# Kernel optimization log

Measured on AMD Instinct MI355X. Metric: run time of the kernel, lower is better.

Reference implementation:

```python
import jax, jax.numpy as jnp
import numpy as np

N_NODES = 100000
N_EDGES = 800000
NUM_GRAPHS = 512
IN_DIM = 16
EDGE_DIM = 1
HID = 64       # emb_dim
MLP_H = 32     # hidden_layers inside each MPNNLayer
L = 3          # num_layers
EPS = 1e-5


def setup_inputs() -> dict:
    key = jax.random.key(0)
    ks = jax.random.split(key, 24)
    s = 0.05
    inp = {
        "x": jax.random.normal(ks[0], (N_NODES, IN_DIM), jnp.float32),
        "edge_index": jax.random.randint(ks[1], (2, N_EDGES), 0, N_NODES),
        "edge_attr": jax.random.uniform(ks[2], (N_EDGES, EDGE_DIM), jnp.float32),
        "batch": jnp.sort(jax.random.randint(ks[3], (N_NODES,), 0, NUM_GRAPHS)),
        # input projection
        "lin_in_w": jax.random.normal(ks[4], (IN_DIM, HID), jnp.float32) * s,
        "lin_in_b": jnp.zeros((HID,), jnp.float32),
        # message MLP (stacked over L layers): Linear(129->32), BN(32), ReLU, Linear(32->64), ReLU, BN(64)
        "msg_w1": jax.random.normal(ks[5], (L, 2 * HID + EDGE_DIM, MLP_H), jnp.float32) * s,
        "msg_b1": jnp.zeros((L, MLP_H), jnp.float32),
        "msg_g1": jnp.ones((L, MLP_H), jnp.float32),
        "msg_be1": jnp.zeros((L, MLP_H), jnp.float32),
        "msg_w2": jax.random.normal(ks[6], (L, MLP_H, HID), jnp.float32) * s,
        "msg_b2": jnp.zeros((L, HID), jnp.float32),
        "msg_g2": jnp.ones((L, HID), jnp.float32),
        "msg_be2": jnp.zeros((L, HID), jnp.float32),
        # update MLP: Linear(128->32), BN(32), ReLU, Linear(32->64), ReLU, BN(64)
        "upd_w1": jax.random.normal(ks[7], (L, 2 * HID, MLP_H), jnp.float32) * s,
        "upd_b1": jnp.zeros((L, MLP_H), jnp.float32),
        "upd_g1": jnp.ones((L, MLP_H), jnp.float32),
        "upd_be1": jnp.zeros((L, MLP_H), jnp.float32),
        "upd_w2": jax.random.normal(ks[8], (L, MLP_H, HID), jnp.float32) * s,
        "upd_b2": jnp.zeros((L, HID), jnp.float32),
        "upd_g2": jnp.ones((L, HID), jnp.float32),
        "upd_be2": jnp.zeros((L, HID), jnp.float32),
        # head Linear(64->1) + ReLU
        "out_w": jax.random.normal(ks[9], (HID, 1), jnp.float32) * s,
        "out_b": jnp.zeros((1,), jnp.float32),
    }
    return inp


def _bn(h, g, b):
    # BatchNorm1d, training-mode batch stats (biased variance), dropout treated as identity (eval)
    mu = jnp.mean(h, axis=0)
    var = jnp.var(h, axis=0)
    return g * (h - mu) * jax.lax.rsqrt(var + EPS) + b


def reference(x, edge_index, edge_attr, batch,
              lin_in_w, lin_in_b,
              msg_w1, msg_b1, msg_g1, msg_be1, msg_w2, msg_b2, msg_g2, msg_be2,
              upd_w1, upd_b1, upd_g1, upd_be1, upd_w2, upd_b2, upd_g2, upd_be2,
              out_w, out_b):
    src = edge_index[0]  # x_j source
    dst = edge_index[1]  # x_i target / aggregation index
    h = x @ lin_in_w + lin_in_b  # [N, HID]
    for l in range(L):
        # message: cat([x_i, x_j, edge_attr]) -> Linear -> BN -> ReLU -> Linear -> ReLU -> BN
        m_in = jnp.concatenate([h[dst], h[src], edge_attr], axis=1)  # [E, 2*HID+EDGE_DIM]
        m = jax.nn.relu(_bn(m_in @ msg_w1[l] + msg_b1[l], msg_g1[l], msg_be1[l]))
        m = _bn(jax.nn.relu(m @ msg_w2[l] + msg_b2[l]), msg_g2[l], msg_be2[l])
        # aggregate: scatter-add over destination nodes
        agg = jax.ops.segment_sum(m, dst, num_segments=N_NODES)  # [N, HID]
        # update: cat([x, aggr]) -> Linear -> BN -> ReLU -> Linear -> ReLU -> BN
        u_in = jnp.concatenate([h, agg], axis=1)  # [N, 2*HID]
        u = jax.nn.relu(_bn(u_in @ upd_w1[l] + upd_b1[l], upd_g1[l], upd_be1[l]))
        u = _bn(jax.nn.relu(u @ upd_w2[l] + upd_b2[l]), upd_g2[l], upd_be2[l])
        h = h + u  # residual (x += conv(...))
    # global mean pool
    pooled = jax.ops.segment_sum(h, batch, num_segments=NUM_GRAPHS)
    counts = jax.ops.segment_sum(jnp.ones((h.shape[0],), h.dtype), batch, num_segments=NUM_GRAPHS)
    pooled = pooled / jnp.maximum(counts, 1.0)[:, None]
    return jax.nn.relu(pooled @ out_w + out_b).reshape(-1)  # [NUM_GRAPHS]
```

## Files before the change

kernel.cpp:

```cpp
#include <hip/hip_runtime.h>
#include <hip/hip_bf16.h>

#define N_NODES   100000
#define N_EDGES   800000
#define NUM_GRAPHS 512
#define IN_DIM    16
#define HID       64
#define MLP_H     32
#define EPS       1e-5f
#define TPB       256
#define SCAN_B    1024
#define NCHUNK    ((N_NODES + SCAN_B - 1) / SCAN_B)
#define GSB       2048
#define NWAVES    (GSB * 4)
#define PER_W     ((N_EDGES + NWAVES - 1) / NWAVES)
#define NODEBLKS  ((N_NODES + 63) / 64)

using nh2   = decltype(__builtin_amdgcn_cvt_pkrtz(0.f, 0.f));
typedef _Float16 f16x8 __attribute__((ext_vector_type(8)));
typedef float    f32x4 __attribute__((ext_vector_type(4)));
typedef int      i32x4 __attribute__((ext_vector_type(4)));

__device__ __forceinline__ nh2 pack2(float a, float b) {
  return __builtin_amdgcn_cvt_pkrtz(a, b);
}
__device__ __forceinline__ float wsum(float v) {
  v += __shfl_xor(v, 1, 64);
  v += __shfl_xor(v, 2, 64);
  v += __shfl_xor(v, 4, 64);
  v += __shfl_xor(v, 8, 64);
  v += __shfl_xor(v, 16, 64);
  v += __shfl_xor(v, 32, 64);
  return v;
}
__device__ __forceinline__ int lbound(const int* __restrict__ rs, int key) {
  int lo = 0, hi = N_NODES;
  while (lo < hi) { int m = (lo + hi) >> 1; if (rs[m] < key) lo = m + 1; else hi = m; }
  return lo;
}

__global__ __launch_bounds__(TPB) void k_deg(const int* __restrict__ ei, int* __restrict__ deg) {
  int e = blockIdx.x * TPB + threadIdx.x;
  if (e < N_EDGES) atomicAdd(&deg[ei[N_EDGES + e]], 1);
}

__global__ __launch_bounds__(SCAN_B) void k_scan_part(const int* __restrict__ deg,
                                                      int* __restrict__ partials) {
  __shared__ int red[SCAN_B];
  int i = blockIdx.x * SCAN_B + threadIdx.x;
  red[threadIdx.x] = (i < N_NODES) ? deg[i] : 0;
  __syncthreads();
  for (int off = SCAN_B / 2; off > 0; off >>= 1) {
    if (threadIdx.x < off) red[threadIdx.x] += red[threadIdx.x + off];
    __syncthreads();
  }
  if (threadIdx.x == 0) partials[blockIdx.x] = red[0];
}

__global__ void k_scan_mid(int* __restrict__ partials, int* __restrict__ row_start) {
  int run = 0;
  for (int b = 0; b < NCHUNK; ++b) { int t = partials[b]; partials[b] = run; run += t; }
  row_start[N_NODES] = run;
}

__global__ __launch_bounds__(SCAN_B) void k_scan_fin(const int* __restrict__ deg,
                                                     const int* __restrict__ partials,
                                                     int* __restrict__ row_start,
                                                     int* __restrict__ cursor) {
  __shared__ int buf[2][SCAN_B];
  int t = threadIdx.x, i = blockIdx.x * SCAN_B + t;
  int v = (i < N_NODES) ? deg[i] : 0;
  buf[0][t] = v;
  __syncthreads();
  int cur = 0;
  for (int off = 1; off < SCAN_B; off <<= 1) {
    int nv = buf[cur][t] + ((t >= off) ? buf[cur][t - off] : 0);
    buf[cur ^ 1][t] = nv; cur ^= 1;
    __syncthreads();
  }
  if (i < N_NODES) {
    int excl = buf[cur][t] - v + partials[blockIdx.x];
    row_start[i] = excl;
    cursor[i] = excl;
  }
}

__global__ __launch_bounds__(TPB) void k_fill(const int* __restrict__ ei,
                                              const float* __restrict__ ea,
                                              int* __restrict__ cursor,
                                              int* __restrict__ srcS,
                                              int* __restrict__ dstS,
                                              float* __restrict__ eaS) {
  int e = blockIdx.x * TPB + threadIdx.x;
  if (e >= N_EDGES) return;
  int dst = ei[N_EDGES + e];
  int pos = atomicAdd(&cursor[dst], 1);
  srcS[pos] = ei[e];
  dstS[pos] = dst;
  eaS[pos] = ea[e];
}

__global__ __launch_bounds__(TPB) void k_lin_in(const float* __restrict__ x,
                                                const float* __restrict__ w,
                                                const float* __restrict__ b,
                                                float* __restrict__ h) {
  int i = blockIdx.x * TPB + threadIdx.x;
  if (i >= N_NODES) return;
  float xi[IN_DIM];
  const float4* xp = reinterpret_cast<const float4*>(x + i * IN_DIM);
#pragma unroll
  for (int q = 0; q < 4; ++q) {
    float4 v = xp[q];
    xi[4*q] = v.x; xi[4*q+1] = v.y; xi[4*q+2] = v.z; xi[4*q+3] = v.w;
  }
  float4* hp = reinterpret_cast<float4*>(h + i * HID);
#pragma unroll
  for (int j4 = 0; j4 < HID/4; ++j4) {
    float o[4];
#pragma unroll
    for (int c = 0; c < 4; ++c) {
      int j = j4*4 + c;
      float acc = b[j];
#pragma unroll
      for (int k = 0; k < IN_DIM; ++k) acc += xi[k] * w[k*HID + j];
      o[c] = acc;
    }
    float4 ov = {o[0], o[1], o[2], o[3]};
    hp[j4] = ov;
  }
}

__global__ __launch_bounds__(TPB) void k_pq(const float* __restrict__ h,
                                            const float* __restrict__ w1,
                                            const float* __restrict__ b1,
                                            float* __restrict__ P,
                                            _Float16* __restrict__ Qh) {
  const int part = __builtin_amdgcn_readfirstlane(threadIdx.x >> 6);
  const int lane = threadIdx.x & 63;
  const int i = blockIdx.x * 64 + lane;
  if (i >= N_NODES) return;
  const int jb = (part & 1) * 16;
  const bool isQ = part >= 2;
  const float* wbase = w1 + (isQ ? 64 * MLP_H : 0) + jb;
  float acc[16];
#pragma unroll
  for (int j = 0; j < 16; ++j) acc[j] = isQ ? 0.f : b1[jb + j];
  const float4* hp = reinterpret_cast<const float4*>(h + i * HID);
#pragma unroll 4
  for (int k4 = 0; k4 < 16; ++k4) {
    float4 a = hp[k4];
    const float* wr = wbase + (k4*4) * MLP_H;
#pragma unroll
    for (int j = 0; j < 16; ++j)
      acc[j] += a.x*wr[j] + a.y*wr[MLP_H+j] + a.z*wr[2*MLP_H+j] + a.w*wr[3*MLP_H+j];
  }
  if (!isQ) {
    float4* pp = reinterpret_cast<float4*>(P + i * MLP_H + jb);
#pragma unroll
    for (int c = 0; c < 4; ++c) {
      float4 o = {acc[4*c], acc[4*c+1], acc[4*c+2], acc[4*c+3]};
      pp[c] = o;
    }
  } else {
    i32x4 o0, o1;
#pragma unroll
    for (int c = 0; c < 4; ++c) {
      o0[c] = __builtin_bit_cast(int, pack2(acc[2*c],     acc[2*c+1]));
      o1[c] = __builtin_bit_cast(int, pack2(acc[8+2*c],   acc[8+2*c+1]));
    }
    i32x4* qp = reinterpret_cast<i32x4*>(Qh + i * MLP_H + jb);
    qp[0] = o0; qp[1] = o1;
  }
}

__global__ __launch_bounds__(TPB) void k_gather(const float* __restrict__ P,
                                                const _Float16* __restrict__ Qh,
                                                const int* __restrict__ srcS,
                                                const int* __restrict__ dstS,
                                                const float* __restrict__ eaS,
                                                const float* __restrict__ w1,
                                                _Float16* __restrict__ z1h,
                                                float* __restrict__ gstat) {
  const int lane = threadIdx.x & 63;
  const int k = lane & 31;
  const int half = lane >> 5;
  const float weak = w1[128 * MLP_H + k];
  float s = 0.f, q = 0.f;
  const int wv = blockIdx.x * 4 + (threadIdx.x >> 6);
  const int c0 = wv * PER_W;
  const int c1 = min(c0 + PER_W, N_EDGES);
  if (c0 < N_EDGES) {
    const int rounds = (c1 - c0 + 1) >> 1;
    const int e0 = c0 + half;
    int ea0 = min(e0, c1 - 1);
    int ea1 = min(e0 + 2, c1 - 1);
    float aA = eaS[ea0], aB = eaS[ea1];
    float qA = (float)Qh[srcS[ea0] * MLP_H + k], qB = (float)Qh[srcS[ea1] * MLP_H + k];
    float pA = P[dstS[ea0] * MLP_H + k], pB = P[dstS[ea1] * MLP_H + k];
    for (int r = 0; r < rounds; ++r) {
      const int ecur = e0 + 2 * r;
      const bool vc = ecur < c1;
      const int ecl = min(ecur, c1 - 1);
      float z = pA + qA + aA * weak;
      pA = pB; qA = qB; aA = aB;
      const int en = min(e0 + 2 * (r + 2), c1 - 1);
      aB = eaS[en]; qB = (float)Qh[srcS[en] * MLP_H + k]; pB = P[dstS[en] * MLP_H + k];
      if (vc) {
        z1h[ecl * MLP_H + k] = (_Float16)z;
        s += z; q = fmaf(z, z, q);
      }
    }
  }
  s += __shfl_xor(s, 32, 64);
  q += __shfl_xor(q, 32, 64);
  __shared__ float ls[4][MLP_H], lq[4][MLP_H];
  const int w = threadIdx.x >> 6;
  if (lane < MLP_H) { ls[w][lane] = s; lq[w][lane] = q; }
  __syncthreads();
  const int t = threadIdx.x;
  if (t < MLP_H)
    unsafeAtomicAdd(&gstat[t], ls[0][t] + ls[1][t] + ls[2][t] + ls[3][t]);
  else if (t < 2*MLP_H)
    unsafeAtomicAdd(&gstat[t], lq[0][t-MLP_H] + lq[1][t-MLP_H] + lq[2][t-MLP_H] + lq[3][t-MLP_H]);
}

__global__ __launch_bounds__(TPB) void k_msgdot(const _Float16* __restrict__ z1h,
                                                const int* __restrict__ rs,
                                                const float* __restrict__ gstat_in,
                                                const float* __restrict__ g1,
                                                const float* __restrict__ be1,
                                                const float* __restrict__ w2,
                                                const float* __restrict__ b2,
                                                float* __restrict__ agg,
                                                float* __restrict__ gstat_out) {
  const int lane = threadIdx.x & 63;
  const int col = lane & 15;
  const int g   = lane >> 4;
  float a1v[8], c1v[8];
#pragma unroll
  for (int i = 0; i < 8; ++i) {
    int kf = g*8 + i;
    float mu = gstat_in[kf] * (1.f / N_EDGES);
    float var = fmaxf(gstat_in[MLP_H + kf] * (1.f / N_EDGES) - mu * mu, 0.f);
    float a = g1[kf] * rsqrtf(var + EPS);
    a1v[i] = a; c1v[i] = be1[kf] - a * mu;
  }
  f16x8 bf0, bf1, bf2, bf3;
#define MKB(BF, C) { i32x4 bw; \
  _Pragma("unroll") for (int ii = 0; ii < 4; ++ii) { \
    nh2 p = pack2(w2[(g*8 + 2*ii) * HID + (C)*16 + col], \
                  w2[(g*8 + 2*ii + 1) * HID + (C)*16 + col]); \
    bw[ii] = __builtin_bit_cast(int, p); } \
  BF = __builtin_bit_cast(f16x8, bw); }
  MKB(bf0, 0) MKB(bf1, 1) MKB(bf2, 2) MKB(bf3, 3)
#undef MKB
  float b2c[4];
#pragma unroll
  for (int c = 0; c < 4; ++c) b2c[c] = b2[c*16 + col];

  float sacc[4] = {0.f,0.f,0.f,0.f}, qacc[4] = {0.f,0.f,0.f,0.f};
  const int wv = blockIdx.x * 4 + (threadIdx.x >> 6);
  const int key0 = min(wv * PER_W, N_EDGES);
  const int key1 = min((wv + 1) * PER_W, N_EDGES);
  const int n0 = lbound(rs, key0);
  const int n1 = (wv == NWAVES - 1) ? N_NODES : lbound(rs, key1);

  for (int n = n0; n < n1; ++n) {
    const int start = rs[n], end = rs[n + 1];
    float aggacc[4] = {0.f,0.f,0.f,0.f};
    for (int t0 = start; t0 < end; t0 += 16) {
      const int ec = min(t0 + col, end - 1);
      f16x8 zv = *reinterpret_cast<const f16x8*>(z1h + ec * MLP_H + g * 8);
      i32x4 aw;
#pragma unroll
      for (int i = 0; i < 4; ++i) {
        float m0 = fmaxf(fmaf(a1v[2*i],   (float)zv[2*i],   c1v[2*i]),   0.f);
        float m1 = fmaxf(fmaf(a1v[2*i+1], (float)zv[2*i+1], c1v[2*i+1]), 0.f);
        aw[i] = __builtin_bit_cast(int, pack2(m0, m1));
      }
      f16x8 af = __builtin_bit_cast(f16x8, aw);
      f32x4 zc = {0.f,0.f,0.f,0.f};
      f32x4 cc0 = __builtin_amdgcn_mfma_f32_16x16x32_f16(af, bf0, zc, 0, 0, 0);
      f32x4 cc1 = __builtin_amdgcn_mfma_f32_16x16x32_f16(af, bf1, zc, 0, 0, 0);
      f32x4 cc2 = __builtin_amdgcn_mfma_f32_16x16x32_f16(af, bf2, zc, 0, 0, 0);
      f32x4 cc3 = __builtin_amdgcn_mfma_f32_16x16x32_f16(af, bf3, zc, 0, 0, 0);
      bool vld[4];
#pragma unroll
      for (int reg = 0; reg < 4; ++reg) vld[reg] = (t0 + g*4 + reg) < end;
#define EPI(CC, CI) { \
  _Pragma("unroll") for (int reg = 0; reg < 4; ++reg) { \
    float tv = fmaxf(CC[reg] + b2c[CI], 0.f); \
    tv = vld[reg] ? tv : 0.f; \
    aggacc[CI] += tv; qacc[CI] = fmaf(tv, tv, qacc[CI]); } }
      EPI(cc0, 0) EPI(cc1, 1) EPI(cc2, 2) EPI(cc3, 3)
#undef EPI
    }
#pragma unroll
    for (int c = 0; c < 4; ++c) sacc[c] += aggacc[c];
#pragma unroll
    for (int c = 0; c < 4; ++c) {
      aggacc[c] += __shfl_xor(aggacc[c], 16, 64);
      aggacc[c] += __shfl_xor(aggacc[c], 32, 64);
    }
    float aout = (g == 0) ? aggacc[0] : (g == 1) ? aggacc[1] : (g == 2) ? aggacc[2] : aggacc[3];
    agg[n * HID + g * 16 + col] = aout;
  }
#pragma unroll
  for (int c = 0; c < 4; ++c) {
    sacc[c] += __shfl_xor(sacc[c], 16, 64);
    sacc[c] += __shfl_xor(sacc[c], 32, 64);
    qacc[c] += __shfl_xor(qacc[c], 16, 64);
    qacc[c] += __shfl_xor(qacc[c], 32, 64);
  }
  __shared__ float ls[4][HID], lq[4][HID];
  const int w = threadIdx.x >> 6;
  if (g == 0) {
#pragma unroll
    for (int c = 0; c < 4; ++c) { ls[w][c*16 + col] = sacc[c]; lq[w][c*16 + col] = qacc[c]; }
  }
  __syncthreads();
  const int t = threadIdx.x;
  if (t < HID)
    unsafeAtomicAdd(&gstat_out[t], ls[0][t] + ls[1][t] + ls[2][t] + ls[3][t]);
  else if (t < 2*HID)
    unsafeAtomicAdd(&gstat_out[t], lq[0][t-HID] + lq[1][t-HID] + lq[2][t-HID] + lq[3][t-HID]);
}

__global__ __launch_bounds__(TPB) void k_upd1(const float* __restrict__ h,
                                              const float* __restrict__ agg,
                                              const int* __restrict__ deg,
                                              const float* __restrict__ gstat_in,
                                              const float* __restrict__ g2,
                                              const float* __restrict__ be2,
                                              const float* __restrict__ w1,
                                              const float* __restrict__ b1,
                                              float* __restrict__ zu1) {
  __shared__ float sa[HID], sc[HID];
  {
    int t = threadIdx.x;
    if (t < HID) {
      float mu = gstat_in[t] * (1.f / N_EDGES);
      float var = fmaxf(gstat_in[HID + t] * (1.f / N_EDGES) - mu * mu, 0.f);
      float a = g2[t] * rsqrtf(var + EPS);
      sa[t] = a; sc[t] = be2[t] - a * mu;
    }
  }
  __syncthreads();
  const int widx = __builtin_amdgcn_readfirstlane(threadIdx.x >> 6);
  const int part = widx & 1;
  const int grp  = blockIdx.x * 2 + (widx >> 1);
  const int lane = threadIdx.x & 63;
  const int jb = part * 16;
  const int i = grp * 64 + lane;
  if (i >= N_NODES) return;
  float acc[16];
#pragma unroll
  for (int j = 0; j < 16; ++j) acc[j] = b1[jb + j];
  const float4* hp = reinterpret_cast<const float4*>(h + i * HID);
#pragma unroll 4
  for (int k4 = 0; k4 < 16; ++k4) {
    float4 a = hp[k4];
    const float* wr = w1 + (k4*4) * MLP_H + jb;
#pragma unroll
    for (int j = 0; j < 16; ++j)
      acc[j] += a.x*wr[j] + a.y*wr[MLP_H+j] + a.z*wr[2*MLP_H+j] + a.w*wr[3*MLP_H+j];
  }
  float degf = (float)deg[i];
  const float4* ap = reinterpret_cast<const float4*>(agg + i * HID);
#pragma unroll 4
  for (int k4 = 0; k4 < 16; ++k4) {
    float4 g4 = ap[k4];
    int k = k4*4;
    float a0 = sa[k]  *g4.x + sc[k]  *degf;
    float a1 = sa[k+1]*g4.y + sc[k+1]*degf;
    float a2 = sa[k+2]*g4.z + sc[k+2]*degf;
    float a3 = sa[k+3]*g4.w + sc[k+3]*degf;
    const float* wr = w1 + (64 + k) * MLP_H + jb;
#pragma unroll
    for (int j = 0; j < 16; ++j)
      acc[j] += a0*wr[j] + a1*wr[MLP_H+j] + a2*wr[2*MLP_H+j] + a3*wr[3*MLP_H+j];
  }
  float4* zp = reinterpret_cast<float4*>(zu1 + i * MLP_H + jb);
#pragma unroll
  for (int c = 0; c < 4; ++c) {
    float4 o = {acc[4*c], acc[4*c+1], acc[4*c+2], acc[4*c+3]};
    zp[c] = o;
  }
}

__global__ __launch_bounds__(TPB) void k_upd2(const float* __restrict__ zu1,
                                              const float* __restrict__ gstat_in,
                                              const float* __restrict__ gu1,
                                              const float* __restrict__ beu1,
                                              const float* __restrict__ w2,
                                              const float* __restrict__ b2,
                                              float* __restrict__ tu) {
  __shared__ float sa[MLP_H], sc[MLP_H];
  {
    int t = threadIdx.x;
    if (t < MLP_H) {
      float mu = gstat_in[t] * (1.f / N_NODES);
      float var = fmaxf(gstat_in[MLP_H + t] * (1.f / N_NODES) - mu * mu, 0.f);
      float a = gu1[t] * rsqrtf(var + EPS);
      sa[t] = a; sc[t] = beu1[t] - a * mu;
    }
  }
  __syncthreads();
  const int widx = __builtin_amdgcn_readfirstlane(threadIdx.x >> 6);
  const int part = widx & 1;
  const int grp  = blockIdx.x * 2 + (widx >> 1);
  const int lane = threadIdx.x & 63;
  const int jb = part * 32;
  const int i = grp * 64 + lane;
  if (i >= N_NODES) return;
  float m1[MLP_H];
  const float4* zp = reinterpret_cast<const float4*>(zu1 + i * MLP_H);
#pragma unroll
  for (int c = 0; c < MLP_H/4; ++c) {
    float4 z = zp[c];
    int kk = 4*c;
    m1[kk]   = fmaxf(sa[kk]  *z.x + sc[kk],   0.f);
    m1[kk+1] = fmaxf(sa[kk+1]*z.y + sc[kk+1], 0.f);
    m1[kk+2] = fmaxf(sa[kk+2]*z.z + sc[kk+2], 0.f);
    m1[kk+3] = fmaxf(sa[kk+3]*z.w + sc[kk+3], 0.f);
  }
#pragma unroll
  for (int j4 = 0; j4 < 8; ++j4) {
    float tv[4];
#pragma unroll
    for (int c = 0; c < 4; ++c) {
      int j = jb + j4*4 + c;
      float v = b2[j];
#pragma unroll
      for (int kk = 0; kk < MLP_H; ++kk) v += m1[kk] * w2[kk*HID + j];
      tv[c] = fmaxf(v, 0.f);
    }
    float4 o = {tv[0], tv[1], tv[2], tv[3]};
    *reinterpret_cast<float4*>(tu + i * HID + jb + j4*4) = o;
  }
}

template <int NF>
__global__ __launch_bounds__(TPB) void k_colstats(const float* __restrict__ X,
                                                  int nrows, float* __restrict__ gstat) {
  const int RPB = TPB / NF;
  int f = threadIdx.x % NF;
  int rloc = threadIdx.x / NF;
  float s = 0.f, q = 0.f;
  for (int r = blockIdx.x * RPB + rloc; r < nrows; r += gridDim.x * RPB) {
    float v = X[r * NF + f];
    s += v; q = fmaf(v, v, q);
  }
  __shared__ float ls[TPB], lq[TPB];
  ls[threadIdx.x] = s; lq[threadIdx.x] = q;
  __syncthreads();
  if (threadIdx.x < NF) {
    float ss = 0.f, qq = 0.f;
#pragma unroll
    for (int r = 0; r < RPB; ++r) { ss += ls[r*NF + f]; qq += lq[r*NF + f]; }
    unsafeAtomicAdd(&gstat[f], ss);
    unsafeAtomicAdd(&gstat[NF + f], qq);
  }
}

__global__ __launch_bounds__(TPB) void k_resid(float* __restrict__ h,
                                               const float* __restrict__ tu,
                                               const float* __restrict__ gstat_in,
                                               const float* __restrict__ gu2,
                                               const float* __restrict__ beu2) {
  __shared__ float sa[HID], sc[HID];
  {
    int t = threadIdx.x;
    if (t < HID) {
      float mu = gstat_in[t] * (1.f / N_NODES);
      float var = fmaxf(gstat_in[HID + t] * (1.f / N_NODES) - mu * mu, 0.f);
      float a = gu2[t] * rsqrtf(var + EPS);
      sa[t] = a; sc[t] = beu2[t] - a * mu;
    }
  }
  __syncthreads();
  int idx = blockIdx.x * TPB + threadIdx.x;
  if (idx >= N_NODES * (HID/4)) return;
  int j0 = (idx & (HID/4 - 1)) * 4;
  float4 hv = reinterpret_cast<const float4*>(h)[idx];
  float4 tv = reinterpret_cast<const float4*>(tu)[idx];
  hv.x += sa[j0]  *tv.x + sc[j0];
  hv.y += sa[j0+1]*tv.y + sc[j0+1];
  hv.z += sa[j0+2]*tv.z + sc[j0+2];
  hv.w += sa[j0+3]*tv.w + sc[j0+3];
  reinterpret_cast<float4*>(h)[idx] = hv;
}

__global__ __launch_bounds__(TPB) void k_pool_head(const float* __restrict__ h,
                                                   const int* __restrict__ batch,
                                                   const float* __restrict__ ow,
                                                   const float* __restrict__ ob,
                                                   float* __restrict__ out) {
  int g = blockIdx.x;
  int lo = 0, hi = N_NODES;
  while (lo < hi) { int mid = (lo+hi) >> 1; if (batch[mid] < g) lo = mid+1; else hi = mid; }
  int start = lo;
  lo = start; hi = N_NODES;
  while (lo < hi) { int mid = (lo+hi) >> 1; if (batch[mid] < g+1) lo = mid+1; else hi = mid; }
  int end = lo;
  int j = threadIdx.x & 63;
  int sub = threadIdx.x >> 6;
  float acc = 0.f;
  for (int n = start + sub; n < end; n += 4) acc += h[n*HID + j];
  __shared__ float red[TPB];
  red[threadIdx.x] = acc;
  __syncthreads();
  if (threadIdx.x < 64) {
    float s = red[threadIdx.x] + red[64+threadIdx.x] + red[128+threadIdx.x] + red[192+threadIdx.x];
    float cnt = (float)(end - start);
    float pooled = s / fmaxf(cnt, 1.0f);
    float v = pooled * ow[threadIdx.x];
    v = wsum(v);
    if (threadIdx.x == 0) out[g] = fmaxf(v + ob[0], 0.f);
  }
}

extern "C" void kernel_launch(void* const* d_in, const int* in_sizes, int n_in,
                              void* d_out, int out_size, void* d_ws, size_t ws_size,
                              hipStream_t stream) {
  const float* x       = (const float*)d_in[0];
  const int*   ei      = (const int*)  d_in[1];
  const float* ea      = (const float*)d_in[2];
  const int*   batch   = (const int*)  d_in[3];
  const float* lin_w   = (const float*)d_in[4];
  const float* lin_b   = (const float*)d_in[5];
  const float* msg_w1  = (const float*)d_in[6];
  const float* msg_b1  = (const float*)d_in[7];
  const float* msg_g1  = (const float*)d_in[8];
  const float* msg_be1 = (const float*)d_in[9];
  const float* msg_w2  = (const float*)d_in[10];
  const float* msg_b2  = (const float*)d_in[11];
  const float* msg_g2  = (const float*)d_in[12];
  const float* msg_be2 = (const float*)d_in[13];
  const float* upd_w1  = (const float*)d_in[14];
  const float* upd_b1  = (const float*)d_in[15];
  const float* upd_g1  = (const float*)d_in[16];
  const float* upd_be1 = (const float*)d_in[17];
  const float* upd_w2  = (const float*)d_in[18];
  const float* upd_b2  = (const float*)d_in[19];
  const float* upd_g2  = (const float*)d_in[20];
  const float* upd_be2 = (const float*)d_in[21];
  const float* out_w   = (const float*)d_in[22];
  const float* out_b   = (const float*)d_in[23];
  float* out = (float*)d_out;

  float* W     = (float*)d_ws;
  float* h     = W;
  float* P     = W + 6400000;
  _Float16* Qh = (_Float16*)(W + 9600000);
  float* agg   = W + 12800000;
  float* z1    = W + 19200000;
  _Float16* z1h = (_Float16*)z1;
  float* zu1   = z1 + 12800000;
  float* tu    = z1 + 16000000;
  float* eaS   = W + 44800000;
  float* stats = W + 45600000;
  int*   ib    = (int*)(W + 45601152);
  int* deg       = ib;
  int* row_start = ib + 100000;
  int* cursor    = ib + 200001;
  int* srcS      = ib + 300001;
  int* dstS      = ib + 1100001;
  int* partials  = ib + 1900001;

  hipMemsetAsync(stats, 0, 3*384*sizeof(float), stream);
  hipMemsetAsync(deg, 0, N_NODES*sizeof(int), stream);

  k_deg<<<N_EDGES/TPB, TPB, 0, stream>>>(ei, deg);
  k_scan_part<<<NCHUNK, SCAN_B, 0, stream>>>(deg, partials);
  k_scan_mid<<<1, 1, 0, stream>>>(partials, row_start);
  k_scan_fin<<<NCHUNK, SCAN_B, 0, stream>>>(deg, partials, row_start, cursor);
  k_fill<<<N_EDGES/TPB, TPB, 0, stream>>>(ei, ea, cursor, srcS, dstS, eaS);

  k_lin_in<<<(N_NODES+TPB-1)/TPB, TPB, 0, stream>>>(x, lin_w, lin_b, h);

  const int PQ_BLKS   = NODEBLKS;
  const int UPD_BLKS  = (NODEBLKS + 1) / 2;

  for (int l = 0; l < 3; ++l) {
    const float* mw1 = msg_w1 + (size_t)l*129*MLP_H;
    const float* mb1 = msg_b1 + l*MLP_H;
    const float* mg1 = msg_g1 + l*MLP_H;
    const float* mbe1= msg_be1 + l*MLP_H;
    const float* mw2 = msg_w2 + (size_t)l*MLP_H*HID;
    const float* mb2 = msg_b2 + l*HID;
    const float* mg2 = msg_g2 + l*HID;
    const float* mbe2= msg_be2 + l*HID;
    const float* uw1 = upd_w1 + (size_t)l*128*MLP_H;
    const float* ub1 = upd_b1 + l*MLP_H;
    const float* ug1 = upd_g1 + l*MLP_H;
    const float* ube1= upd_be1 + l*MLP_H;
    const float* uw2 = upd_w2 + (size_t)l*MLP_H*HID;
    const float* ub2 = upd_b2 + l*HID;
    const float* ug2 = upd_g2 + l*HID;
    const float* ube2= upd_be2 + l*HID;
    float* st = stats + l*384;

    k_pq<<<PQ_BLKS, TPB, 0, stream>>>(h, mw1, mb1, P, Qh);
    k_gather<<<GSB, TPB, 0, stream>>>(P, Qh, srcS, dstS, eaS, mw1, z1h, st);
    k_msgdot<<<GSB, TPB, 0, stream>>>(z1h, row_start, st, mg1, mbe1, mw2, mb2, agg, st+64);
    k_upd1<<<UPD_BLKS, TPB, 0, stream>>>(h, agg, deg, st+64, mg2, mbe2, uw1, ub1, zu1);
    k_colstats<MLP_H><<<512, TPB, 0, stream>>>(zu1, N_NODES, st+192);
    k_upd2<<<UPD_BLKS, TPB, 0, stream>>>(zu1, st+192, ug1, ube1, uw2, ub2, tu);
    k_colstats<HID><<<512, TPB, 0, stream>>>(tu, N_NODES, st+256);
    k_resid<<<(N_NODES*(HID/4)+TPB-1)/TPB, TPB, 0, stream>>>(h, tu, st+256, ug2, ube2);
  }

  k_pool_head<<<NUM_GRAPHS, TPB, 0, stream>>>(h, batch, out_w, out_b, out);
}
```

Before: 1.001 ms.

## Pack sorted edge records into int4 and process four edges per wave in gather

Replaces the three separate sorted arrays (src, dst, edge attr) with one 16-byte record per edge, so each gather step issues a single vector load for the edge metadata. The gather kernel now has each lane handle two feature columns, with 16 lanes per edge and four edges per wave step. It reads packed half2 values of Q and float2 values of P, writes packed half2 outputs, and prefetches records three steps ahead. This cuts the number of load and store instructions and the dependent index loads. The cost is more record storage (one padding word per edge) and extra shuffle reductions for the statistics.

```diff
diff --git a/kernel.cpp b/kernel.cpp
--- a/kernel.cpp
+++ b/kernel.cpp
@@ -88,16 +88,17 @@
 __global__ __launch_bounds__(TPB) void k_fill(const int* __restrict__ ei,
                                               const float* __restrict__ ea,
                                               int* __restrict__ cursor,
-                                              int* __restrict__ srcS,
-                                              int* __restrict__ dstS,
-                                              float* __restrict__ eaS) {
+                                              i32x4* __restrict__ erec) {
   int e = blockIdx.x * TPB + threadIdx.x;
   if (e >= N_EDGES) return;
   int dst = ei[N_EDGES + e];
   int pos = atomicAdd(&cursor[dst], 1);
-  srcS[pos] = ei[e];
-  dstS[pos] = dst;
-  eaS[pos] = ea[e];
+  i32x4 rec;
+  rec[0] = ei[e];
+  rec[1] = dst;
+  rec[2] = __float_as_int(ea[e]);
+  rec[3] = 0;
+  erec[pos] = rec;
 }
 
 __global__ __launch_bounds__(TPB) void k_lin_in(const float* __restrict__ x,
@@ -175,47 +176,64 @@
 
 __global__ __launch_bounds__(TPB) void k_gather(const float* __restrict__ P,
                                                 const _Float16* __restrict__ Qh,
-                                                const int* __restrict__ srcS,
-                                                const int* __restrict__ dstS,
-                                                const float* __restrict__ eaS,
+                                                const i32x4* __restrict__ erec,
                                                 const float* __restrict__ w1,
                                                 _Float16* __restrict__ z1h,
                                                 float* __restrict__ gstat) {
   const int lane = threadIdx.x & 63;
-  const int k = lane & 31;
-  const int half = lane >> 5;
-  const float weak = w1[128 * MLP_H + k];
-  float s = 0.f, q = 0.f;
+  const int kq  = lane & 15;
+  const int qtr = lane >> 4;
+  const float wk0 = w1[128 * MLP_H + 2*kq];
+  const float wk1 = w1[128 * MLP_H + 2*kq + 1];
+  const int* Qi = (const int*)Qh;
+  int* z1i = (int*)z1h;
+  float s0 = 0.f, s1 = 0.f, qa0 = 0.f, qa1 = 0.f;
   const int wv = blockIdx.x * 4 + (threadIdx.x >> 6);
   const int c0 = wv * PER_W;
   const int c1 = min(c0 + PER_W, N_EDGES);
   if (c0 < N_EDGES) {
-    const int rounds = (c1 - c0 + 1) >> 1;
-    const int e0 = c0 + half;
-    int ea0 = min(e0, c1 - 1);
-    int ea1 = min(e0 + 2, c1 - 1);
-    float aA = eaS[ea0], aB = eaS[ea1];
-    float qA = (float)Qh[srcS[ea0] * MLP_H + k], qB = (float)Qh[srcS[ea1] * MLP_H + k];
-    float pA = P[dstS[ea0] * MLP_H + k], pB = P[dstS[ea1] * MLP_H + k];
+    const int c1m1 = c1 - 1;
+    const int rounds = (c1 - c0 + 3) >> 2;
+#define EIDX(R) min(c0 + 4*(R) + qtr, c1m1)
+    i32x4 rec2 = erec[EIDX(0)];
+    i32x4 rec3 = erec[EIDX(1)];
+    i32x4 recH = erec[EIDX(2)];
+    int   qiA = Qi[rec2[0] * 16 + kq];
+    float2 pA = *reinterpret_cast<const float2*>(P + rec2[1] * MLP_H + 2*kq);
+    float  aA = __int_as_float(rec2[2]);
+    int   qiB = Qi[rec3[0] * 16 + kq];
+    float2 pB = *reinterpret_cast<const float2*>(P + rec3[1] * MLP_H + 2*kq);
+    float  aB = __int_as_float(rec3[2]);
     for (int r = 0; r < rounds; ++r) {
-      const int ecur = e0 + 2 * r;
-      const bool vc = ecur < c1;
-      const int ecl = min(ecur, c1 - 1);
-      float z = pA + qA + aA * weak;
-      pA = pB; qA = qB; aA = aB;
-      const int en = min(e0 + 2 * (r + 2), c1 - 1);
-      aB = eaS[en]; qB = (float)Qh[srcS[en] * MLP_H + k]; pB = P[dstS[en] * MLP_H + k];
-      if (vc) {
-        z1h[ecl * MLP_H + k] = (_Float16)z;
-        s += z; q = fmaf(z, z, q);
+      i32x4 recN = erec[EIDX(r + 3)];
+      int   qiC = Qi[recH[0] * 16 + kq];
+      float2 pC = *reinterpret_cast<const float2*>(P + recH[1] * MLP_H + 2*kq);
+      float  aC = __int_as_float(recH[2]);
+      const int e = c0 + 4*r + qtr;
+      nh2 hv = __builtin_bit_cast(nh2, qiA);
+      float z0 = pA.x + (float)hv.x + aA * wk0;
+      float z1 = pA.y + (float)hv.y + aA * wk1;
+      if (e < c1) {
+        z1i[min(e, c1m1) * 16 + kq] = __builtin_bit_cast(int, pack2(z0, z1));
+        s0 += z0; s1 += z1;
+        qa0 = fmaf(z0, z0, qa0); qa1 = fmaf(z1, z1, qa1);
       }
-    }
-  }
-  s += __shfl_xor(s, 32, 64);
-  q += __shfl_xor(q, 32, 64);
+      qiA = qiB; pA = pB; aA = aB;
+      qiB = qiC; pB = pC; aB = aC;
+      recH = recN;
+    }
+#undef EIDX
+  }
+  s0  += __shfl_xor(s0, 16, 64);  s0  += __shfl_xor(s0, 32, 64);
+  s1  += __shfl_xor(s1, 16, 64);  s1  += __shfl_xor(s1, 32, 64);
+  qa0 += __shfl_xor(qa0, 16, 64); qa0 += __shfl_xor(qa0, 32, 64);
+  qa1 += __shfl_xor(qa1, 16, 64); qa1 += __shfl_xor(qa1, 32, 64);
   __shared__ float ls[4][MLP_H], lq[4][MLP_H];
   const int w = threadIdx.x >> 6;
-  if (lane < MLP_H) { ls[w][lane] = s; lq[w][lane] = q; }
+  if (lane < 16) {
+    ls[w][2*lane] = s0; ls[w][2*lane+1] = s1;
+    lq[w][2*lane] = qa0; lq[w][2*lane+1] = qa1;
+  }
   __syncthreads();
   const int t = threadIdx.x;
   if (t < MLP_H)
@@ -554,19 +572,16 @@
   float* P     = W + 6400000;
   _Float16* Qh = (_Float16*)(W + 9600000);
   float* agg   = W + 12800000;
-  float* z1    = W + 19200000;
-  _Float16* z1h = (_Float16*)z1;
-  float* zu1   = z1 + 12800000;
-  float* tu    = z1 + 16000000;
-  float* eaS   = W + 44800000;
-  float* stats = W + 45600000;
-  int*   ib    = (int*)(W + 45601152);
+  _Float16* z1h = (_Float16*)(W + 19200000);
+  float* zu1   = W + 32000000;
+  float* tu    = W + 35200000;
+  float* stats = W + 41600000;
+  int*   ib    = (int*)(W + 41601152);
   int* deg       = ib;
   int* row_start = ib + 100000;
   int* cursor    = ib + 200001;
-  int* srcS      = ib + 300001;
-  int* dstS      = ib + 1100001;
-  int* partials  = ib + 1900001;
+  int* partials  = ib + 300001;
+  i32x4* erec    = (i32x4*)(ib + 300232);
 
   hipMemsetAsync(stats, 0, 3*384*sizeof(float), stream);
   hipMemsetAsync(deg, 0, N_NODES*sizeof(int), stream);
@@ -575,7 +590,7 @@
   k_scan_part<<<NCHUNK, SCAN_B, 0, stream>>>(deg, partials);
   k_scan_mid<<<1, 1, 0, stream>>>(partials, row_start);
   k_scan_fin<<<NCHUNK, SCAN_B, 0, stream>>>(deg, partials, row_start, cursor);
-  k_fill<<<N_EDGES/TPB, TPB, 0, stream>>>(ei, ea, cursor, srcS, dstS, eaS);
+  k_fill<<<N_EDGES/TPB, TPB, 0, stream>>>(ei, ea, cursor, erec);
 
   k_lin_in<<<(N_NODES+TPB-1)/TPB, TPB, 0, stream>>>(x, lin_w, lin_b, h);
 
@@ -602,7 +617,7 @@
     float* st = stats + l*384;
 
     k_pq<<<PQ_BLKS, TPB, 0, stream>>>(h, mw1, mb1, P, Qh);
-    k_gather<<<GSB, TPB, 0, stream>>>(P, Qh, srcS, dstS, eaS, mw1, z1h, st);
+    k_gather<<<GSB, TPB, 0, stream>>>(P, Qh, erec, mw1, z1h, st);
     k_msgdot<<<GSB, TPB, 0, stream>>>(z1h, row_start, st, mg1, mbe1, mw2, mb2, agg, st+64);
     k_upd1<<<UPD_BLKS, TPB, 0, stream>>>(h, agg, deg, st+64, mg2, mbe2, uw1, ub1, zu1);
     k_colstats<MLP_H><<<512, TPB, 0, stream>>>(zu1, N_NODES, st+192);
```

Result: faster. 964.2 us (-3.6%).
